# Performance work log

Measured on AMD Instinct MI355X. Metric: run time of the kernel, lower is better.

Reference implementation:

```python
import jax, jax.numpy as jnp
import numpy as np
from jax import lax

NUM_LAYERS = 8
K = 3
C = 128  # residual/gate/skip channels
DIL_H = (1, 2, 4, 8, 1, 2, 4, 8)
DIL_W = (1, 2, 4, 8, 16, 32, 64, 128)
DN = ('NCHW', 'OIHW', 'NCHW')


def _conv(x, w, b, dh=1, dw=1, pad_h=0, pad_w=0):
    # causal along H: pad only on top by pad_h (equivalent to pytorch's
    # symmetric pad + out[:, :, :-pad_h] slice); symmetric along W.
    out = lax.conv_general_dilated(
        x, w, window_strides=(1, 1),
        padding=((pad_h, 0), (pad_w, pad_w)),
        rhs_dilation=(dh, dw), dimension_numbers=DN)
    return out + b[None, :, None, None]


def setup_inputs() -> dict:
    key = jax.random.key(0)
    ks = jax.random.split(key, 6)
    B, H, W = 2, 16, 4096
    return {
        'x': jax.random.normal(ks[0], (B, 1, H, W), jnp.float32),
        'c': jax.random.normal(ks[1], (B, 80, H, W), jnp.float32),
        'front_w': jax.random.normal(ks[2], (C, 1, 1, 1), jnp.float32),
        'front_b': jnp.zeros((C,), jnp.float32),
        'fg_w': jax.random.normal(ks[3], (NUM_LAYERS, 2 * C, C, K, K), jnp.float32) * (1.0 / np.sqrt(C * K * K)),
        'fg_b': jnp.zeros((NUM_LAYERS, 2 * C), jnp.float32),
        'fgc_w': jax.random.normal(ks[4], (NUM_LAYERS, 2 * C, 80, 1, 1), jnp.float32) * (1.0 / np.sqrt(80)),
        'fgc_b': jnp.zeros((NUM_LAYERS, 2 * C), jnp.float32),
        'rs_w': jax.random.normal(ks[5], (NUM_LAYERS, 2 * C, C, 1, 1), jnp.float32) * (1.0 / np.sqrt(C)),
        'rs_b': jnp.zeros((NUM_LAYERS, 2 * C), jnp.float32),
    }


def reference(x, c, front_w, front_b, fg_w, fg_b, fgc_w, fgc_b, rs_w, rs_b):
    # front 1x1 conv (causal but pad_h = 0 for kernel_size=1)
    h = _conv(x, front_w, front_b)  # [B, C, H, W]
    skip = jnp.zeros_like(h)
    for i in range(NUM_LAYERS):
        dh, dw = DIL_H[i], DIL_W[i]
        pad_h = dh * (K - 1)
        pad_w = dw * (K - 1) // 2
        # dilated causal conv -> [B, 2C, H, W]
        hg = _conv(h, fg_w[i], fg_b[i], dh, dw, pad_h, pad_w)
        # 1x1 conditioning conv on c
        cg = _conv(c, fgc_w[i], fgc_b[i])
        a = hg + cg
        acts = jnp.tanh(a[:, :C]) * jax.nn.sigmoid(a[:, C:])
        # 1x1 res/skip conv -> [B, 2C, H, W]
        rs = _conv(acts, rs_w[i], rs_b[i])
        h = h + rs[:, :C]
        skip = skip + rs[:, C:]
    return skip
```

## Files before the change

### kernel.cpp

```cpp
#include <hip/hip_runtime.h>
#include <math.h>

#define NL    8
#define CCH   128
#define CINC  80
#define CPAD  128
#define HH    16
#define WW    4096
#define HW    (HH*WW)
#define PADW  128
#define WWP   (WW + 2*PADW)
#define NT    10
#define PADF  64

#define HF32_N  (2*HW*CCH)
#define HBF_N   (2*HH*WWP*CCH)
#define ZROW_N  (WWP*CCH)
#define CT_N    (2*HW*CPAD)
#define GW_N    (NL*NT*4*16*64*8)
#define RW_N    (NL*4*16*64*8)

using v8s   = __attribute__((ext_vector_type(8))) short;
using f32x4 = __attribute__((ext_vector_type(4))) float;

__device__ __forceinline__ unsigned short f2bf(float f) {
    unsigned int u = __builtin_bit_cast(unsigned int, f);
    u += 0x7fffu + ((u >> 16) & 1u);
    return (unsigned short)(u >> 16);
}
__device__ __forceinline__ float sigm(float x) { return 1.0f / (1.0f + __expf(-x)); }

__device__ __forceinline__ void gl_lds16(const void* g, void* l) {
    __builtin_amdgcn_global_load_lds(
        (const __attribute__((address_space(1))) unsigned int*)g,
        (__attribute__((address_space(3))) unsigned int*)l, 16, 0, 0);
}

__global__ void prep_weights(const float* __restrict__ fg_w, const float* __restrict__ fgc_w,
                             const float* __restrict__ rs_w,
                             const float* __restrict__ fg_b, const float* __restrict__ fgc_b,
                             const float* __restrict__ rs_b,
                             unsigned short* __restrict__ gw, unsigned short* __restrict__ rw,
                             float* __restrict__ gbias, float* __restrict__ rbias) {
    const int total = GW_N + RW_N + 2 * NL * 256;
    const int stride = gridDim.x * blockDim.x;
    for (int idx = blockIdx.x * blockDim.x + threadIdx.x; idx < total; idx += stride) {
        if (idx < GW_N) {
            int t0 = idx;
            int j = t0 & 7;  t0 >>= 3;
            int l = t0 & 63; t0 >>= 6;
            int mt = t0 & 15; t0 >>= 4;
            int tq = t0 % (NT*4);
            int i  = t0 / (NT*4);
            int t  = tq >> 2, q = tq & 3;
            int m  = mt*16 + (l & 15);
            int oo = (m & 1)*128 + (m >> 1);
            int ci = q*32 + 8*(l >> 4) + j;
            float v;
            if (t < 9) {
                v = fg_w[(((size_t)i*256 + oo)*128 + ci)*9 + t];
            } else {
                v = (ci < CINC) ? fgc_w[((size_t)i*256 + oo)*CINC + ci] : 0.0f;
            }
            gw[idx] = f2bf(v);
        } else if (idx < GW_N + RW_N) {
            int t0 = idx - GW_N;
            int j = t0 & 7;  t0 >>= 3;
            int l = t0 & 63; t0 >>= 6;
            int mt = t0 & 15; t0 >>= 4;
            int q = t0 & 3;
            int i = t0 >> 2;
            int m  = mt*16 + (l & 15);
            int oo = (m & 1)*128 + (m >> 1);
            int ci = q*32 + 8*(l >> 4) + j;
            rw[idx - GW_N] = f2bf(rs_w[((size_t)i*256 + oo)*128 + ci]);
        } else {
            int t0 = idx - GW_N - RW_N;
            if (t0 < NL*256) {
                int i = t0 >> 8, m = t0 & 255;
                int oo = (m & 1)*128 + (m >> 1);
                gbias[t0] = fg_b[i*256 + oo] + fgc_b[i*256 + oo];
            } else {
                t0 -= NL*256;
                int i = t0 >> 8, m = t0 & 255;
                int oo = (m & 1)*128 + (m >> 1);
                rbias[t0] = rs_b[i*256 + oo];
            }
        }
    }
}

__global__ void front_kernel(const float* __restrict__ xsrc,
                             const float* __restrict__ fw, const float* __restrict__ fb,
                             float* __restrict__ hf32, unsigned short* __restrict__ hbf0,
                             unsigned short* __restrict__ hbf1, unsigned short* __restrict__ zrow) {
    const int stride = gridDim.x * blockDim.x;
    const int t0 = blockIdx.x * blockDim.x + threadIdx.x;
    for (int idx = t0; idx < HF32_N; idx += stride) {
        int x = idx & (WW - 1);
        int y = (idx >> 12) & 15;
        int c = (idx >> 16) & 127;
        int b = idx >> 23;
        hf32[idx] = fw[c] * xsrc[((size_t)(b*HH + y))*WW + x] + fb[c];
    }
    for (int idx = t0; idx < HBF_N; idx += stride) {
        int c = idx & 127;
        int rest = idx >> 7;
        int xp = rest % WWP; rest /= WWP;
        int y = rest & 15;
        int b = rest >> 4;
        int x = xp - PADW;
        if (x >= 0 && x < WW)
            hbf0[idx] = f2bf(fw[c] * xsrc[((size_t)(b*HH + y))*WW + x] + fb[c]);
        else
            hbf0[idx] = 0;
    }
    const int PADN = 2*HH*2*PADW*CCH;
    for (int idx = t0; idx < PADN; idx += stride) {
        int c = idx & 127;
        int r = idx >> 7;
        int xo = r % (2*PADW); r /= (2*PADW);
        int y = r & 15;
        int b = r >> 4;
        int xp = (xo < PADW) ? xo : xo + WW;
        hbf1[(((size_t)(b*HH + y))*WWP + xp)*CCH + c] = 0;
    }
    for (int idx = t0; idx < ZROW_N; idx += stride) zrow[idx] = 0;
}

__global__ __launch_bounds__(256) void cond_transpose(const float* __restrict__ cin,
                                                      unsigned short* __restrict__ cT) {
    __shared__ unsigned short lt[CINC][72];
    const int tid = threadIdx.x, lane = tid & 63, w = tid >> 6;
    const int x0 = blockIdx.x * 64, y = blockIdx.y, b = blockIdx.z;
#pragma unroll
    for (int r = 0; r < 20; ++r) {
        int ci = w*20 + r;
        float v = cin[(((size_t)(b*CINC + ci))*HH + y)*WW + x0 + lane];
        lt[ci][lane] = f2bf(v);
    }
    __syncthreads();
    const int px = tid & 63, cg = tid >> 6;
    unsigned int pk[16];
#pragma unroll
    for (int kk = 0; kk < 16; ++kk) {
        int c0 = cg*32 + kk*2;
        unsigned int lo = (c0     < CINC) ? lt[c0][px]     : 0;
        unsigned int hi = (c0 + 1 < CINC) ? lt[c0 + 1][px] : 0;
        pk[kk] = lo | (hi << 16);
    }
    unsigned short* dst = cT + (((size_t)(b*HH + y))*WW + x0 + px)*CPAD + cg*32;
#pragma unroll
    for (int u = 0; u < 4; ++u)
        *(uint4*)(dst + u*8) = make_uint4(pk[u*4], pk[u*4+1], pk[u*4+2], pk[u*4+3]);
}

__global__ __launch_bounds__(256, 3) void layer_fused(
        const unsigned short* __restrict__ hin, unsigned short* __restrict__ hout,
        const unsigned short* __restrict__ zrow, const unsigned short* __restrict__ cT,
        const unsigned short* __restrict__ gw, const float* __restrict__ gbias,
        const unsigned short* __restrict__ rw, const float* __restrict__ rbias,
        float* __restrict__ hf32, float* __restrict__ outskip,
        int layer, int dh, int dw, int first) {
    __shared__ char sbuf[2 * 16384];

    const int tid = threadIdx.x, lane = tid & 63, w = tid >> 6;
    const int lrow = lane & 15, lk = lane >> 4;

    const int lin = blockIdx.x + 64*(blockIdx.y + 16*blockIdx.z);
    const int logical = (lin & 7)*256 + (lin >> 3);
    const int x0 = (logical & 63) * 64;
    const int y  = (logical >> 6) & 15;
    const int b  = logical >> 10;

    f32x4 acc[4][4];
#pragma unroll
    for (int mf = 0; mf < 4; ++mf)
#pragma unroll
        for (int nf = 0; nf < 4; ++nf) acc[mf][nf] = (f32x4){0.f, 0.f, 0.f, 0.f};

    const unsigned short* rowb[3];
#pragma unroll
    for (int kh = 0; kh < 3; ++kh) {
        int yin = y - (2 - kh)*dh;
        rowb[kh] = (yin >= 0) ? hin + ((size_t)(b*HH + yin))*WWP*CCH : zrow;
    }
    const char* cb = (const char*)(cT + (((size_t)(b*HH + y))*WW + x0)*CPAD);
    const unsigned short* gwl = gw + (((size_t)layer*NT*4*16) + w*4)*512 + lane*8;

    auto stage = [&](char* dst, const char* src) {
#pragma unroll
        for (int s = 0; s < 4; ++s) {
            unsigned o = (unsigned)(w*4 + s)*1024 + (unsigned)lane*16;
            unsigned g = o ^ (((o >> 8) & 7) << 4);
            gl_lds16(src + g, dst + (w*4 + s)*1024);
        }
    };
    auto stage_t = [&](int t) {
        const char* src;
        if (t == 9) src = cb;
        else {
            int kh = t / 3, kw = t - kh*3;
            src = (const char*)(rowb[kh] + (size_t)(x0 + (kw - 1)*dw + PADW)*CCH);
        }
        stage(sbuf + (t & 1)*16384, src);
    };
    auto dsread = [&](const char* bb, int q, v8s (&bv)[4]) {
#pragma unroll
        for (int nf = 0; nf < 4; ++nf) {
            int px = nf*16 + lrow;
            int o = px*256 + ((q*64 + lk*16) ^ ((lrow & 7) << 4));
            bv[nf] = *(const v8s*)(bb + o);
        }
    };
    auto loadA = [&](int t, int q, v8s (&av)[4]) {
        const unsigned short* gq = gwl + (size_t)(t*4 + q)*16*512;
#pragma unroll
        for (int mf = 0; mf < 4; ++mf) av[mf] = *(const v8s*)(gq + mf*512);
    };
    auto mf16 = [&](v8s (&av)[4], v8s (&bv)[4]) {
        __builtin_amdgcn_s_setprio(1);
#pragma unroll
        for (int mf = 0; mf < 4; ++mf)
#pragma unroll
            for (int nf = 0; nf < 4; ++nf)
                acc[mf][nf] = __builtin_amdgcn_mfma_f32_16x16x32_bf16(av[mf], bv[nf], acc[mf][nf], 0, 0, 0);
        __builtin_amdgcn_s_setprio(0);
    };

    v8s aA[4], aB[4], bv[4];
    stage_t(0);
    loadA(0, 0, aA);
    loadA(0, 1, aB);
#pragma unroll
    for (int t = 0; t < NT; ++t) {
        asm volatile("s_waitcnt vmcnt(8)" ::: "memory");
        __builtin_amdgcn_sched_barrier(0);
        __builtin_amdgcn_s_barrier();
        __builtin_amdgcn_sched_barrier(0);
        if (t + 1 < NT) stage_t(t + 1);
        const char* bb = sbuf + (t & 1)*16384;
        dsread(bb, 0, bv); mf16(aA, bv); loadA(t, 2, aA);
        dsread(bb, 1, bv); mf16(aB, bv); loadA(t, 3, aB);
        dsread(bb, 2, bv); mf16(aA, bv); if (t + 1 < NT) loadA(t + 1, 0, aA);
        dsread(bb, 3, bv); mf16(aB, bv); if (t + 1 < NT) loadA(t + 1, 1, aB);
    }

    char* sact = sbuf;
    const float* gb = gbias + layer*256;
#pragma unroll
    for (int mf = 0; mf < 4; ++mf) {
        int m0 = w*64 + mf*16 + lk*4;
        int c0 = m0 >> 1;
        float bF0 = gb[m0], bG0 = gb[m0+1], bF1 = gb[m0+2], bG1 = gb[m0+3];
#pragma unroll
        for (int nf = 0; nf < 4; ++nf) {
            int px = nf*16 + lrow;
            float o0 = tanhf(acc[mf][nf][0] + bF0) * sigm(acc[mf][nf][1] + bG0);
            float o1 = tanhf(acc[mf][nf][2] + bF1) * sigm(acc[mf][nf][3] + bG1);
            unsigned int pk = (unsigned int)f2bf(o0) | ((unsigned int)f2bf(o1) << 16);
            int byte = px*256 + c0*2;
            byte ^= (px & 7) << 4;
            *(unsigned int*)(sact + byte) = pk;
        }
    }
#pragma unroll
    for (int mf = 0; mf < 4; ++mf)
#pragma unroll
        for (int nf = 0; nf < 4; ++nf) acc[mf][nf] = (f32x4){0.f, 0.f, 0.f, 0.f};
    __syncthreads();

    const unsigned short* rwl = rw + (((size_t)layer*4*16) + w*4)*512 + lane*8;
#pragma unroll
    for (int q = 0; q < 4; ++q) {
        v8s av[4];
#pragma unroll
        for (int mf = 0; mf < 4; ++mf) av[mf] = *(const v8s*)(rwl + (size_t)(q*16 + mf)*512);
        dsread(sact, q, bv);
        __builtin_amdgcn_s_setprio(1);
#pragma unroll
        for (int mf = 0; mf < 4; ++mf)
#pragma unroll
            for (int nf = 0; nf < 4; ++nf)
                acc[mf][nf] = __builtin_amdgcn_mfma_f32_16x16x32_bf16(av[mf], bv[nf], acc[mf][nf], 0, 0, 0);
        __builtin_amdgcn_s_setprio(0);
    }
    __syncthreads();

    float* sresf = (float*)sbuf;
    const int cp = tid >> 4, xg = tid & 15;
    const int pxl = tid & 63, cg = tid >> 6;

    if (layer < NL - 1) {
#pragma unroll
        for (int mf = 0; mf < 4; ++mf) {
            int c0 = w*32 + mf*8 + lk*2;
#pragma unroll
            for (int nf = 0; nf < 4; ++nf) {
                int px = nf*16 + lrow;
                sresf[(c0    )*PADF + px] = acc[mf][nf][0];
                sresf[(c0 + 1)*PADF + px] = acc[mf][nf][2];
            }
        }
        __syncthreads();
#pragma unroll
        for (int it = 0; it < 8; ++it) {
            int cc = it*16 + cp;
            float4 r = *(float4*)(sresf + cc*PADF + xg*4);
            size_t p = (((size_t)(b*CCH + cc))*HH + y)*WW + x0 + xg*4;
            float4 h = *(const float4*)(hf32 + p);
            float bb2 = rbias[layer*256 + 2*cc];
            h.x += r.x + bb2; h.y += r.y + bb2; h.z += r.z + bb2; h.w += r.w + bb2;
            *(float4*)(hf32 + p) = h;
            *(float4*)(sresf + cc*PADF + xg*4) = h;
        }
        __syncthreads();
        {
            unsigned int pk3[16];
#pragma unroll
            for (int j = 0; j < 16; ++j) {
                float lo = sresf[(cg*32 + 2*j    )*PADF + pxl];
                float hi = sresf[(cg*32 + 2*j + 1)*PADF + pxl];
                pk3[j] = (unsigned int)f2bf(lo) | ((unsigned int)f2bf(hi) << 16);
            }
            unsigned short* hrow = hout + (((size_t)(b*HH + y))*WWP + x0 + pxl + PADW)*CCH + cg*32;
#pragma unroll
            for (int u = 0; u < 4; ++u)
                *(uint4*)(hrow + u*8) = make_uint4(pk3[u*4], pk3[u*4+1], pk3[u*4+2], pk3[u*4+3]);
        }
        __syncthreads();
    }

#pragma unroll
    for (int mf = 0; mf < 4; ++mf) {
        int c0 = w*32 + mf*8 + lk*2;
#pragma unroll
        for (int nf = 0; nf < 4; ++nf) {
            int px = nf*16 + lrow;
            sresf[(c0    )*PADF + px] = acc[mf][nf][1];
            sresf[(c0 + 1)*PADF + px] = acc[mf][nf][3];
        }
    }
    __syncthreads();
#pragma unroll
    for (int it = 0; it < 8; ++it) {
        int cc = it*16 + cp;
        float4 s = *(float4*)(sresf + cc*PADF + xg*4);
        float bb2 = rbias[layer*256 + 2*cc + 1];
        s.x += bb2; s.y += bb2; s.z += bb2; s.w += bb2;
        size_t p = (((size_t)(b*CCH + cc))*HH + y)*WW + x0 + xg*4;
        if (first) {
            *(float4*)(outskip + p) = s;
        } else {
            float4 o = *(const float4*)(outskip + p);
            o.x += s.x; o.y += s.y; o.z += s.z; o.w += s.w;
            *(float4*)(outskip + p) = o;
        }
    }
}

extern "C" void kernel_launch(void* const* d_in, const int* in_sizes, int n_in,
                              void* d_out, int out_size, void* d_ws, size_t ws_size,
                              hipStream_t stream) {
    const float* x       = (const float*)d_in[0];
    const float* c       = (const float*)d_in[1];
    const float* front_w = (const float*)d_in[2];
    const float* front_b = (const float*)d_in[3];
    const float* fg_w    = (const float*)d_in[4];
    const float* fg_b    = (const float*)d_in[5];
    const float* fgc_w   = (const float*)d_in[6];
    const float* fgc_b   = (const float*)d_in[7];
    const float* rs_w    = (const float*)d_in[8];
    const float* rs_b    = (const float*)d_in[9];

    char* ws = (char*)d_ws;
    float* hf32   = (float*)ws;                     ws += (size_t)HF32_N * 4;
    unsigned short* hbf0 = (unsigned short*)ws;     ws += (size_t)HBF_N * 2;
    unsigned short* hbf1 = (unsigned short*)ws;     ws += (size_t)HBF_N * 2;
    unsigned short* zrow = (unsigned short*)ws;     ws += (size_t)ZROW_N * 2;
    unsigned short* cT   = (unsigned short*)ws;     ws += (size_t)CT_N * 2;
    unsigned short* gw   = (unsigned short*)ws;     ws += (size_t)GW_N * 2;
    unsigned short* rwq  = (unsigned short*)ws;     ws += (size_t)RW_N * 2;
    float* gbias  = (float*)ws;                     ws += (size_t)NL * 256 * 4;
    float* rbias  = (float*)ws;

    float* outp = (float*)d_out;

    prep_weights<<<2048, 256, 0, stream>>>(fg_w, fgc_w, rs_w, fg_b, fgc_b, rs_b,
                                           gw, rwq, gbias, rbias);
    front_kernel<<<2048, 256, 0, stream>>>(x, front_w, front_b, hf32, hbf0, hbf1, zrow);
    cond_transpose<<<dim3(64, 16, 2), 256, 0, stream>>>(c, cT);

    static const int DILH[NL] = {1, 2, 4, 8, 1, 2, 4, 8};
    static const int DILW[NL] = {1, 2, 4, 8, 16, 32, 64, 128};

    for (int i = 0; i < NL; ++i) {
        const unsigned short* hin = (i & 1) ? hbf1 : hbf0;
        unsigned short*       hout= (i & 1) ? hbf0 : hbf1;
        layer_fused<<<dim3(64, 16, 2), 256, 0, stream>>>(hin, hout, zrow, cT, gw, gbias,
                                                         rwq, rbias, hf32, outp,
                                                         i, DILH[i], DILW[i], i == 0 ? 1 : 0);
    }
}
```

Baseline: 1.024 ms.

## Drop fp32 residual buffer; read residual from staged bf16 center tap in LDS

Removes the fp32 copy of the residual state h and its per-layer global read-modify-write. The tap order is changed so the conditioning tile is staged at slot 7 and the center tap (kh=2, kw=1) is staged last, leaving it resident in LDS. Its bf16 values are then reused as the residual input to h + rs. This saves global traffic and one sync, but the residual stream now accumulates in bf16 across layers, which loses precision and risks tolerance failures.

```diff
diff --git a/kernel.cpp b/kernel.cpp
--- a/kernel.cpp
+++ b/kernel.cpp
@@ -13,7 +13,6 @@
 #define NT    10
 #define PADF  64
 
-#define HF32_N  (2*HW*CCH)
 #define HBF_N   (2*HH*WWP*CCH)
 #define ZROW_N  (WWP*CCH)
 #define CT_N    (2*HW*CPAD)
@@ -35,6 +34,8 @@
         (const __attribute__((address_space(1))) unsigned int*)g,
         (__attribute__((address_space(3))) unsigned int*)l, 16, 0, 0);
 }
+
+__device__ __host__ __forceinline__ int tap_of(int t) { return (t < 7) ? t : (t == 8 ? 8 : 7); }
 
 __global__ void prep_weights(const float* __restrict__ fg_w, const float* __restrict__ fgc_w,
                              const float* __restrict__ rs_w,
@@ -57,10 +58,11 @@
             int oo = (m & 1)*128 + (m >> 1);
             int ci = q*32 + 8*(l >> 4) + j;
             float v;
-            if (t < 9) {
-                v = fg_w[(((size_t)i*256 + oo)*128 + ci)*9 + t];
+            if (t == 7) {
+                v = (ci < CINC) ? fgc_w[((size_t)i*256 + oo)*CINC + ci] : 0.0f;
             } else {
-                v = (ci < CINC) ? fgc_w[((size_t)i*256 + oo)*CINC + ci] : 0.0f;
+                int tt = tap_of(t);
+                v = fg_w[(((size_t)i*256 + oo)*128 + ci)*9 + tt];
             }
             gw[idx] = f2bf(v);
         } else if (idx < GW_N + RW_N) {
@@ -92,17 +94,10 @@
 
 __global__ void front_kernel(const float* __restrict__ xsrc,
                              const float* __restrict__ fw, const float* __restrict__ fb,
-                             float* __restrict__ hf32, unsigned short* __restrict__ hbf0,
+                             unsigned short* __restrict__ hbf0,
                              unsigned short* __restrict__ hbf1, unsigned short* __restrict__ zrow) {
     const int stride = gridDim.x * blockDim.x;
     const int t0 = blockIdx.x * blockDim.x + threadIdx.x;
-    for (int idx = t0; idx < HF32_N; idx += stride) {
-        int x = idx & (WW - 1);
-        int y = (idx >> 12) & 15;
-        int c = (idx >> 16) & 127;
-        int b = idx >> 23;
-        hf32[idx] = fw[c] * xsrc[((size_t)(b*HH + y))*WW + x] + fb[c];
-    }
     for (int idx = t0; idx < HBF_N; idx += stride) {
         int c = idx & 127;
         int rest = idx >> 7;
@@ -160,7 +155,7 @@
         const unsigned short* __restrict__ zrow, const unsigned short* __restrict__ cT,
         const unsigned short* __restrict__ gw, const float* __restrict__ gbias,
         const unsigned short* __restrict__ rw, const float* __restrict__ rbias,
-        float* __restrict__ hf32, float* __restrict__ outskip,
+        float* __restrict__ outskip,
         int layer, int dh, int dw, int first) {
     __shared__ char sbuf[2 * 16384];
 
@@ -198,9 +193,10 @@
     };
     auto stage_t = [&](int t) {
         const char* src;
-        if (t == 9) src = cb;
+        if (t == 7) src = cb;
         else {
-            int kh = t / 3, kw = t - kh*3;
+            int tt = tap_of(t);
+            int kh = tt / 3, kw = tt - kh*3;
             src = (const char*)(rowb[kh] + (size_t)(x0 + (kw - 1)*dw + PADW)*CCH);
         }
         stage(sbuf + (t & 1)*16384, src);
@@ -285,6 +281,20 @@
                 acc[mf][nf] = __builtin_amdgcn_mfma_f32_16x16x32_bf16(av[mf], bv[nf], acc[mf][nf], 0, 0, 0);
         __builtin_amdgcn_s_setprio(0);
     }
+
+    unsigned int hold[4][4];
+    if (layer < NL - 1) {
+#pragma unroll
+        for (int mf = 0; mf < 4; ++mf) {
+            int c0 = w*32 + mf*8 + lk*2;
+#pragma unroll
+            for (int nf = 0; nf < 4; ++nf) {
+                int px = nf*16 + lrow;
+                int o = px*256 + ((c0*2) ^ ((px & 7) << 4));
+                hold[mf][nf] = *(const unsigned int*)(sbuf + 16384 + o);
+            }
+        }
+    }
     __syncthreads();
 
     float* sresf = (float*)sbuf;
@@ -295,24 +305,16 @@
 #pragma unroll
         for (int mf = 0; mf < 4; ++mf) {
             int c0 = w*32 + mf*8 + lk*2;
+            float bR0 = rbias[layer*256 + 2*c0];
+            float bR1 = rbias[layer*256 + 2*(c0 + 1)];
 #pragma unroll
             for (int nf = 0; nf < 4; ++nf) {
                 int px = nf*16 + lrow;
-                sresf[(c0    )*PADF + px] = acc[mf][nf][0];
-                sresf[(c0 + 1)*PADF + px] = acc[mf][nf][2];
+                float h0 = __builtin_bit_cast(float, (hold[mf][nf] & 0xffffu) << 16);
+                float h1 = __builtin_bit_cast(float, hold[mf][nf] & 0xffff0000u);
+                sresf[(c0    )*PADF + px] = h0 + acc[mf][nf][0] + bR0;
+                sresf[(c0 + 1)*PADF + px] = h1 + acc[mf][nf][2] + bR1;
             }
-        }
-        __syncthreads();
-#pragma unroll
-        for (int it = 0; it < 8; ++it) {
-            int cc = it*16 + cp;
-            float4 r = *(float4*)(sresf + cc*PADF + xg*4);
-            size_t p = (((size_t)(b*CCH + cc))*HH + y)*WW + x0 + xg*4;
-            float4 h = *(const float4*)(hf32 + p);
-            float bb2 = rbias[layer*256 + 2*cc];
-            h.x += r.x + bb2; h.y += r.y + bb2; h.z += r.z + bb2; h.w += r.w + bb2;
-            *(float4*)(hf32 + p) = h;
-            *(float4*)(sresf + cc*PADF + xg*4) = h;
         }
         __syncthreads();
         {
@@ -374,7 +376,6 @@
     const float* rs_b    = (const float*)d_in[9];
 
     char* ws = (char*)d_ws;
-    float* hf32   = (float*)ws;                     ws += (size_t)HF32_N * 4;
     unsigned short* hbf0 = (unsigned short*)ws;     ws += (size_t)HBF_N * 2;
     unsigned short* hbf1 = (unsigned short*)ws;     ws += (size_t)HBF_N * 2;
     unsigned short* zrow = (unsigned short*)ws;     ws += (size_t)ZROW_N * 2;
@@ -388,7 +389,7 @@
 
     prep_weights<<<2048, 256, 0, stream>>>(fg_w, fgc_w, rs_w, fg_b, fgc_b, rs_b,
                                            gw, rwq, gbias, rbias);
-    front_kernel<<<2048, 256, 0, stream>>>(x, front_w, front_b, hf32, hbf0, hbf1, zrow);
+    front_kernel<<<2048, 256, 0, stream>>>(x, front_w, front_b, hbf0, hbf1, zrow);
     cond_transpose<<<dim3(64, 16, 2), 256, 0, stream>>>(c, cT);
 
     static const int DILH[NL] = {1, 2, 4, 8, 1, 2, 4, 8};
@@ -398,7 +399,7 @@
         const unsigned short* hin = (i & 1) ? hbf1 : hbf0;
         unsigned short*       hout= (i & 1) ? hbf0 : hbf1;
         layer_fused<<<dim3(64, 16, 2), 256, 0, stream>>>(hin, hout, zrow, cT, gw, gbias,
-                                                         rwq, rbias, hf32, outp,
+                                                         rwq, rbias, outp,
                                                          i, DILH[i], DILW[i], i == 0 ? 1 : 0);
     }
 }
```

After: 904.0 us. 1.13x faster.
